# Kernel optimization log

Hardware: AMD Instinct MI355X
Metric: run time of the kernel (lower is better)

## Reference

```python
import jax, jax.numpy as jnp
import numpy as np
import math

N_HEADS = 4
N_ITERS = 2  # SSFormer n=2; each loop iteration recomputes the same values (no feedback in the original code)
BN_EPS = 1e-5


def _attention(q, k, v):
    """SSTransformer: multi-head cross-attention over flattened spatial dims.
    q,k,v: [B, C, H, W] -> returns [B, C, L] with L = H*W.
    """
    b, c = q.shape[0], q.shape[1]
    L = q.shape[2] * q.shape[3]
    ch = c // N_HEADS
    scale = 1.0 / math.sqrt(math.sqrt(ch))
    qf = (q.reshape(b * N_HEADS, ch, L) * scale)
    kf = (k.reshape(b * N_HEADS, ch, L) * scale)
    vf = v.reshape(b * N_HEADS, ch, L)
    # weight: [B*H, t, s]
    w = jnp.einsum('bct,bcs->bts', qf, kf)
    w = jax.nn.softmax(w.astype(jnp.float32), axis=-1).astype(w.dtype)
    a = jnp.einsum('bts,bcs->bct', w, vf)
    return a.reshape(b, c, L)


def setup_inputs() -> dict:
    key = jax.random.key(0)
    k1, k2, k3, k4 = jax.random.split(key, 4)
    B, C, H, W = 8, 512, 32, 32
    c = jax.random.normal(k1, (B, C, H, W), dtype=jnp.float32)
    e = jax.random.normal(k2, (B, C, H, W), dtype=jnp.float32)
    conv_w = jax.random.normal(k3, (C, C, 1, 1), dtype=jnp.float32) / math.sqrt(C)
    conv_b = jax.random.normal(k4, (C,), dtype=jnp.float32) * 0.02
    bn_gamma = jnp.ones((C,), dtype=jnp.float32)
    bn_beta = jnp.zeros((C,), dtype=jnp.float32)
    return {"c": c, "e": e, "conv_w": conv_w, "conv_b": conv_b,
            "bn_gamma": bn_gamma, "bn_beta": bn_beta}


def reference(c, e, conv_w, conv_b, bn_gamma, bn_beta):
    bs, ch, h, w = c.shape
    L = h * w
    for _ in range(N_ITERS):
        _c = _attention(e, c, c)                       # [B, C, L]
        _e = _attention(_c.reshape(bs, ch, h, w), e, e)  # [B, C, L]
    _e = _e.reshape(bs, ch, h, w)
    # Proj: 1x1 conv + BatchNorm2d (training-mode batch stats) + Swish
    x = jnp.einsum('oc,bchw->bohw', conv_w.reshape(ch, ch), _e) + conv_b[None, :, None, None]
    mean = jnp.mean(x, axis=(0, 2, 3), keepdims=True)
    var = jnp.var(x, axis=(0, 2, 3), keepdims=True)
    xn = (x - mean) * jax.lax.rsqrt(var + BN_EPS)
    xn = xn * bn_gamma[None, :, None, None] + bn_beta[None, :, None, None]
    return xn * jax.nn.sigmoid(xn)
```

## Files before the change

### kernel.cpp

```cpp
#include <hip/hip_runtime.h>
#include <hip/hip_bf16.h>

typedef __attribute__((ext_vector_type(8))) short short8;
typedef __attribute__((ext_vector_type(4))) float floatx4;
typedef __attribute__((ext_vector_type(4))) float f32x4;
typedef unsigned short u16;
typedef unsigned int u32;
typedef __attribute__((ext_vector_type(8))) unsigned short ushort8;

#define LSEQ 1024
#define CHD  128
#define QK_SCALE 0.08838834764831845f

static __device__ __forceinline__ u16 f2b(float f) {
  __hip_bfloat16 h = __float2bfloat16(f);
  return *reinterpret_cast<u16*>(&h);
}
static __device__ __forceinline__ u32 pack2(float a, float b) {
  return (u32)f2b(a) | ((u32)f2b(b) << 16);
}
static __device__ __forceinline__ void gl_lds16(const void* g, void* l) {
  __builtin_amdgcn_global_load_lds((__attribute__((address_space(1))) const void*)g,
                                   (__attribute__((address_space(3))) void*)l, 16, 0, 0);
}

__global__ __launch_bounds__(256) void k_prep(const float* __restrict__ in,
                                              u16* __restrict__ outV,
                                              u16* __restrict__ outT) {
  __shared__ u16 tile[32][72];
  int bh = blockIdx.z, c0 = blockIdx.y * 32, s0 = blockIdx.x * 64;
  int tid = threadIdx.x;
  int cl = tid >> 3, sc = tid & 7;
  size_t off = ((size_t)bh * CHD + c0 + cl) * LSEQ + s0 + sc * 8;
  f32x4 a = *(const f32x4*)(in + off);
  f32x4 b = *(const f32x4*)(in + off + 4);
  ushort8 u;
#pragma unroll
  for (int j = 0; j < 4; ++j) { u[j] = f2b(a[j]); u[j + 4] = f2b(b[j]); }
  *(ushort8*)(outV + off) = u;
  *(ushort8*)&tile[cl][sc * 8] = u;
  __syncthreads();
  int sl = tid >> 2, cc = tid & 3;
  ushort8 v;
#pragma unroll
  for (int j = 0; j < 8; ++j) v[j] = tile[cc * 8 + j][sl];
  *(ushort8*)(outT + ((size_t)bh * LSEQ + s0 + sl) * CHD + c0 + cc * 8) = v;
}

__global__ __launch_bounds__(256) void k_wcvt(const float* __restrict__ w, u16* __restrict__ wb,
                                              float* __restrict__ zbuf ) {
  int tid = threadIdx.x;
  int base = (blockIdx.x * 256 + tid) * 8;
  f32x4 a = *(const f32x4*)(w + base);
  f32x4 b = *(const f32x4*)(w + base + 4);
  ushort8 u;
#pragma unroll
  for (int j = 0; j < 4; ++j) { u[j] = f2b(a[j]); u[j + 4] = f2b(b[j]); }
  *(ushort8*)(wb + base) = u;
  if (blockIdx.x == 0) {
    f32x4 z; z[0]=0.f; z[1]=0.f; z[2]=0.f; z[3]=0.f;
    *(f32x4*)(zbuf + tid * 4) = z;
  }
}

__global__ __launch_bounds__(512) void k_attn(const u16* __restrict__ qT,
                                              const u16* __restrict__ kT,
                                              const u16* __restrict__ v,
                                              u16* __restrict__ outT) {
  __shared__ char ldsbuf[81920];

  int bh = blockIdx.x, tt = blockIdx.y;
  int tid = threadIdx.x;
  int w = tid >> 6, lane = tid & 63;
  int lo = lane & 15, hi = lane >> 4;
  int t0 = tt * 128 + w * 16;

  const char* kTb = (const char*)(kT + (size_t)bh * LSEQ * CHD);
  const char* vb  = (const char*)(v  + (size_t)bh * CHD * LSEQ);

  const u16* qbase = qT + ((size_t)bh * LSEQ + t0 + lo) * CHD + hi * 8;
  short8 bq[4];
#pragma unroll
  for (int ks = 0; ks < 4; ++ks) bq[ks] = *(const short8*)(qbase + ks * 32);

  floatx4 oacc[8];
#pragma unroll
  for (int i = 0; i < 8; ++i) { oacc[i][0]=0.f; oacc[i][1]=0.f; oacc[i][2]=0.f; oacc[i][3]=0.f; }
  float m_r = -1e30f, l_r = 0.f;

  char* pw = ldsbuf + 65536 + w * 2048 + lo * 128;
  int sw = (lo & 7) << 4;

  auto stageK = [&](int buf, int sb) {
    char* dst = ldsbuf + buf * 16384;
#pragma unroll
    for (int it = 0; it < 2; ++it) {
      int bb = it * 8192 + tid * 16;
      int row = bb >> 8;
      int cb = (bb & 255) ^ ((row & 7) << 4);
      gl_lds16(kTb + (size_t)(sb * 64 + row) * 256 + cb, dst + bb);
    }
  };
  auto stageV = [&](int buf, int sb) {
    char* dst = ldsbuf + 32768 + buf * 16384;
#pragma unroll
    for (int it = 0; it < 2; ++it) {
      int bb = it * 8192 + tid * 16;
      int row = bb >> 7;
      int cb = (bb & 127) ^ ((row & 7) << 4);
      gl_lds16(vb + (size_t)row * 2048 + sb * 128 + cb, dst + bb);
    }
  };

  stageK(0, 0); stageV(0, 0);
  __syncthreads();
  int cur = 0;

  for (int sb = 0; sb < 16; ++sb) {
    if (sb < 15) { stageK(cur ^ 1, sb + 1); stageV(cur ^ 1, sb + 1); }
    const char* ldsK = ldsbuf + cur * 16384;
    const char* ldsV = ldsbuf + 32768 + cur * 16384;

    float sa[4][4];
#pragma unroll
    for (int ss = 0; ss < 4; ++ss) {
      floatx4 acc; acc[0]=0.f; acc[1]=0.f; acc[2]=0.f; acc[3]=0.f;
      int row = ss * 16 + lo;
#pragma unroll
      for (int ks = 0; ks < 4; ++ks) {
        int cbyte = (ks * 64 + hi * 16) ^ ((row & 7) << 4);
        short8 a = *(const short8*)(ldsK + row * 256 + cbyte);
        acc = __builtin_amdgcn_mfma_f32_16x16x32_bf16(a, bq[ks], acc, 0, 0, 0);
      }
#pragma unroll
      for (int r = 0; r < 4; ++r) sa[ss][r] = acc[r] * QK_SCALE;
    }

    float bm = sa[0][0];
#pragma unroll
    for (int ss = 0; ss < 4; ++ss)
#pragma unroll
      for (int r = 0; r < 4; ++r) bm = fmaxf(bm, sa[ss][r]);
    bm = fmaxf(bm, __shfl_xor(bm, 16));
    bm = fmaxf(bm, __shfl_xor(bm, 32));
    float mn = fmaxf(m_r, bm);
    float corr = __expf(m_r - mn);
    m_r = mn;
    float rs = 0.f;
#pragma unroll
    for (int ss = 0; ss < 4; ++ss)
#pragma unroll
      for (int r = 0; r < 4; ++r) {
        float p = __expf(sa[ss][r] - mn);
        sa[ss][r] = p;
        rs += p;
      }
    rs += __shfl_xor(rs, 16);
    rs += __shfl_xor(rs, 32);
    l_r = l_r * corr + rs;
#pragma unroll
    for (int i = 0; i < 8; ++i) {
      oacc[i][0] *= corr; oacc[i][1] *= corr; oacc[i][2] *= corr; oacc[i][3] *= corr;
    }

#pragma unroll
    for (int ss = 0; ss < 4; ++ss)
#pragma unroll
      for (int r2 = 0; r2 < 2; ++r2) {
        int scol = ss * 16 + hi * 4 + r2 * 2;
        *(u32*)(pw + ((scol * 2) ^ sw)) = pack2(sa[ss][r2 * 2], sa[ss][r2 * 2 + 1]);
      }
    asm volatile("" ::: "memory");

#pragma unroll
    for (int mt = 0; mt < 8; ++mt) {
      int crow = mt * 16 + lo;
      const char* va = ldsV + crow * 128;
      int vsw = (crow & 7) << 4;
#pragma unroll
      for (int k2 = 0; k2 < 2; ++k2) {
        short8 a = *(const short8*)(va + ((k2 * 64 + hi * 16) ^ vsw));
        short8 b = *(const short8*)(pw + ((k2 * 64 + hi * 16) ^ sw));
        oacc[mt] = __builtin_amdgcn_mfma_f32_16x16x32_bf16(a, b, oacc[mt], 0, 0, 0);
      }
    }
    __syncthreads();
    cur ^= 1;
  }

  float inv = 1.0f / l_r;
  char* ot = ldsbuf + w * 4096;
#pragma unroll
  for (int mt = 0; mt < 8; ++mt)
#pragma unroll
    for (int r2 = 0; r2 < 2; ++r2) {
      int cb = (mt * 32 + hi * 8 + r2 * 4) ^ ((lo & 7) << 4);
      *(u32*)(ot + lo * 256 + cb) = pack2(oacc[mt][r2 * 2] * inv, oacc[mt][r2 * 2 + 1] * inv);
    }
  asm volatile("" ::: "memory");
  u16* orow = outT + ((size_t)bh * LSEQ + t0 + lo) * CHD;
#pragma unroll
  for (int it = 0; it < 4; ++it) {
    int cb = (it * 64 + hi * 16) ^ ((lo & 7) << 4);
    ushort8 d = *(const ushort8*)(ot + lo * 256 + cb);
    *(ushort8*)(orow + it * 32 + hi * 8) = d;
  }
}

__global__ __launch_bounds__(256) void k_proj(const u16* __restrict__ Wm,
                                              const u16* __restrict__ eT,
                                              const float* __restrict__ bias,
                                              float* __restrict__ x,
                                              float* __restrict__ chsum,
                                              float* __restrict__ chsq) {
  __shared__ char lds[65536];
  int lt = blockIdx.x, ot = blockIdx.y;
  int b = lt >> 3;
  int l0b = (lt & 7) * 128;
  int o0 = ot * 128;
  int tid = threadIdx.x, w = tid >> 6, lane = tid & 63, lo = lane & 15, hi = lane >> 4;
  int wm = w >> 1, wn = w & 1;
  const char* Wb = (const char*)Wm;
  const char* eTb = (const char*)eT;

  auto stageA = [&](int buf, int kb) {
    char* dst = lds + buf * 16384;
#pragma unroll
    for (int it = 0; it < 4; ++it) {
      int bb = it * 4096 + tid * 16;
      int row = bb >> 7;
      int cb = (bb & 127) ^ ((row & 7) << 4);
      gl_lds16(Wb + (size_t)(o0 + row) * 1024 + kb * 128 + cb, dst + bb);
    }
  };
  auto stageB = [&](int buf, int kb) {
    char* dst = lds + 32768 + buf * 16384;
    int page = b * 4 + (kb >> 1);
    int choff = (kb & 1) * 128;
#pragma unroll
    for (int it = 0; it < 4; ++it) {
      int bb = it * 4096 + tid * 16;
      int row = bb >> 7;
      int cb = (bb & 127) ^ ((row & 7) << 4);
      gl_lds16(eTb + ((size_t)page * 1024 + l0b + row) * 256 + choff + cb, dst + bb);
    }
  };

  floatx4 acc[4][4];
#pragma unroll
  for (int i = 0; i < 4; ++i)
#pragma unroll
    for (int j = 0; j < 4; ++j) { acc[i][j][0]=0.f; acc[i][j][1]=0.f; acc[i][j][2]=0.f; acc[i][j][3]=0.f; }

  stageA(0, 0); stageB(0, 0);
  __syncthreads();
  int cur = 0;

  for (int kb = 0; kb < 8; ++kb) {
    if (kb < 7) { stageA(cur ^ 1, kb + 1); stageB(cur ^ 1, kb + 1); }
    const char* A = lds + cur * 16384;
    const char* B = lds + 32768 + cur * 16384;
#pragma unroll
    for (int kk = 0; kk < 2; ++kk) {
      short8 af[4], bf[4];
#pragma unroll
      for (int mi = 0; mi < 4; ++mi) {
        int row = wm * 64 + mi * 16 + lo;
        af[mi] = *(const short8*)(A + row * 128 + ((kk * 64 + hi * 16) ^ ((row & 7) << 4)));
      }
#pragma unroll
      for (int ni = 0; ni < 4; ++ni) {
        int row = wn * 64 + ni * 16 + lo;
        bf[ni] = *(const short8*)(B + row * 128 + ((kk * 64 + hi * 16) ^ ((row & 7) << 4)));
      }
#pragma unroll
      for (int mi = 0; mi < 4; ++mi)
#pragma unroll
        for (int ni = 0; ni < 4; ++ni)
          acc[mi][ni] = __builtin_amdgcn_mfma_f32_16x16x32_bf16(af[mi], bf[ni], acc[mi][ni], 0, 0, 0);
    }
    __syncthreads();
    cur ^= 1;
  }

#pragma unroll
  for (int mi = 0; mi < 4; ++mi) {
#pragma unroll
    for (int r = 0; r < 4; ++r) {
      int o = o0 + wm * 64 + mi * 16 + hi * 4 + r;
      float bv = bias[o];
      float s = 0.f, q = 0.f;
#pragma unroll
      for (int ni = 0; ni < 4; ++ni) {
        float xv = acc[mi][ni][r] + bv;
        x[((size_t)b * 512 + o) * LSEQ + l0b + wn * 64 + ni * 16 + lo] = xv;
        s += xv; q += xv * xv;
      }
#pragma unroll
      for (int d = 1; d < 16; d <<= 1) { s += __shfl_xor(s, d); q += __shfl_xor(q, d); }
      if (lo == 0) {
        atomicAdd(&chsum[o], s);
        atomicAdd(&chsq[o], q);
      }
    }
  }
}

__global__ void k_stats(const float* __restrict__ chsum, const float* __restrict__ chsq,
                        const float* __restrict__ gamma, const float* __restrict__ beta,
                        float* __restrict__ scale, float* __restrict__ shift) {
  int ch = blockIdx.x * 256 + threadIdx.x;
  if (ch < 512) {
    const float invn = 1.0f / 8192.0f;
    float mean = chsum[ch] * invn;
    float var = chsq[ch] * invn - mean * mean;
    float rstd = rsqrtf(var + 1e-5f);
    float g = gamma[ch] * rstd;
    scale[ch] = g;
    shift[ch] = beta[ch] - mean * g;
  }
}

__global__ __launch_bounds__(256) void k_final(const float* __restrict__ x,
                                               const float* __restrict__ scale,
                                               const float* __restrict__ shift,
                                               float* __restrict__ out) {
  int idx = blockIdx.x * 256 + threadIdx.x;
  int base = idx * 4;
  int ch = (base >> 10) & 511;
  float sc = scale[ch], sh = shift[ch];
  f32x4 vx = *(const f32x4*)(x + base);
  f32x4 o;
#pragma unroll
  for (int j = 0; j < 4; ++j) {
    float xn = vx[j] * sc + sh;
    float sg = 1.0f / (1.0f + __expf(-xn));
    o[j] = xn * sg;
  }
  *(f32x4*)(out + base) = o;
}

extern "C" void kernel_launch(void* const* d_in, const int* in_sizes, int n_in,
                              void* d_out, int out_size, void* d_ws, size_t ws_size,
                              hipStream_t stream) {
  const float* c     = (const float*)d_in[0];
  const float* e     = (const float*)d_in[1];
  const float* Wf    = (const float*)d_in[2];
  const float* bias  = (const float*)d_in[3];
  const float* gamma = (const float*)d_in[4];
  const float* beta  = (const float*)d_in[5];
  float* outp = (float*)d_out;

  char* ws = (char*)d_ws;
  const size_t TB = (size_t)32 * 1024 * 128 * 2;
  u16* eT  = (u16*)(ws);
  u16* cT  = (u16*)(ws + TB);
  u16* cV  = (u16*)(ws + 2 * TB);
  u16* eV  = (u16*)(ws + 3 * TB);
  u16* cT2 = (u16*)(ws + 4 * TB);
  u16* Wbf = (u16*)(ws + 5 * TB);
  float* chsum = (float*)(ws + 5 * TB + (1 << 20));
  float* chsq  = chsum + 512;
  float* scale = chsq + 512;
  float* shift = scale + 512;
  float* x     = (float*)(ws + 2 * TB);

  dim3 tb(256);
  dim3 pgrid(16, 4, 32);
  dim3 agrid(32, 8);

  k_wcvt<<<dim3(128), tb, 0, stream>>>(Wf, Wbf, chsum);
  k_prep<<<pgrid, tb, 0, stream>>>(c, cV, cT);
  k_prep<<<pgrid, tb, 0, stream>>>(e, eV, eT);
  k_attn<<<agrid, dim3(512), 0, stream>>>(eT, cT, cV, cT2);
  k_attn<<<agrid, dim3(512), 0, stream>>>(cT2, eT, eV, cT);
  k_proj<<<dim3(64, 4), tb, 0, stream>>>(Wbf, cT, bias, x, chsum, chsq);
  k_stats<<<dim3(2), tb, 0, stream>>>(chsum, chsq, gamma, beta, scale, shift);
  k_final<<<dim3(4096), tb, 0, stream>>>(x, scale, shift, outp);
}
```

Baseline: 116.5 us.

## Fuse both attention passes into one kernel and merge prep and stats launches

Both cross-attention passes now run inside one kernel. Each block keeps the first pass's normalized output in LDS and reuses it directly as the query of the second pass, since the query rows it needs are exactly the ones it just produced. This removes a global round-trip and a launch. Blocks shrink from 512 to 256 threads with 64 query rows each, giving twice as many blocks. The two prep launches are merged into one grid, the stats kernel is folded into the final elementwise kernel (every thread recomputes its channel's scale and shift), and s_setprio hints are added around the MFMA sections. The tradeoff is fewer queries per block, so each K/V tile staged from global memory is shared by fewer rows, plus a serial dependency between the two passes inside each block.

Measured after the change: 119.1 us. 1.02x slower.

```diff
diff --git a/kernel.cpp b/kernel.cpp
--- a/kernel.cpp
+++ b/kernel.cpp
@@ -24,11 +24,16 @@
                                    (__attribute__((address_space(3))) void*)l, 16, 0, 0);
 }
 
-__global__ __launch_bounds__(256) void k_prep(const float* __restrict__ in,
-                                              u16* __restrict__ outV,
-                                              u16* __restrict__ outT) {
+__global__ __launch_bounds__(256) void k_prep(const float* __restrict__ cin,
+                                              const float* __restrict__ ein,
+                                              u16* __restrict__ cV, u16* __restrict__ cT,
+                                              u16* __restrict__ eV, u16* __restrict__ eT) {
   __shared__ u16 tile[32][72];
-  int bh = blockIdx.z, c0 = blockIdx.y * 32, s0 = blockIdx.x * 64;
+  int z = blockIdx.z;
+  const float* in = (z < 32) ? cin : ein;
+  u16* outV = (z < 32) ? cV : eV;
+  u16* outT = (z < 32) ? cT : eT;
+  int bh = z & 31, c0 = blockIdx.y * 32, s0 = blockIdx.x * 64;
   int tid = threadIdx.x;
   int cl = tid >> 3, sc = tid & 7;
   size_t off = ((size_t)bh * CHD + c0 + cl) * LSEQ + s0 + sc * 8;
@@ -63,130 +68,159 @@
   }
 }
 
-__global__ __launch_bounds__(512) void k_attn(const u16* __restrict__ qT,
-                                              const u16* __restrict__ kT,
-                                              const u16* __restrict__ v,
+__global__ __launch_bounds__(256) void k_attn(const u16* __restrict__ eT,
+                                              const u16* __restrict__ cT,
+                                              const u16* __restrict__ cV,
+                                              const u16* __restrict__ eV,
                                               u16* __restrict__ outT) {
-  __shared__ char ldsbuf[81920];
+  __shared__ char ldsbuf[73728];
 
   int bh = blockIdx.x, tt = blockIdx.y;
   int tid = threadIdx.x;
   int w = tid >> 6, lane = tid & 63;
   int lo = lane & 15, hi = lane >> 4;
-  int t0 = tt * 128 + w * 16;
-
-  const char* kTb = (const char*)(kT + (size_t)bh * LSEQ * CHD);
-  const char* vb  = (const char*)(v  + (size_t)bh * CHD * LSEQ);
-
-  const u16* qbase = qT + ((size_t)bh * LSEQ + t0 + lo) * CHD + hi * 8;
-  short8 bq[4];
-#pragma unroll
-  for (int ks = 0; ks < 4; ++ks) bq[ks] = *(const short8*)(qbase + ks * 32);
-
-  floatx4 oacc[8];
-#pragma unroll
-  for (int i = 0; i < 8; ++i) { oacc[i][0]=0.f; oacc[i][1]=0.f; oacc[i][2]=0.f; oacc[i][3]=0.f; }
-  float m_r = -1e30f, l_r = 0.f;
+  int t0 = tt * 64 + w * 16;
 
   char* pw = ldsbuf + 65536 + w * 2048 + lo * 128;
   int sw = (lo & 7) << 4;
 
-  auto stageK = [&](int buf, int sb) {
+  auto stageK = [&](int buf, int sb, const char* kTb) {
     char* dst = ldsbuf + buf * 16384;
 #pragma unroll
-    for (int it = 0; it < 2; ++it) {
-      int bb = it * 8192 + tid * 16;
+    for (int it = 0; it < 4; ++it) {
+      int bb = it * 4096 + tid * 16;
       int row = bb >> 8;
       int cb = (bb & 255) ^ ((row & 7) << 4);
       gl_lds16(kTb + (size_t)(sb * 64 + row) * 256 + cb, dst + bb);
     }
   };
-  auto stageV = [&](int buf, int sb) {
+  auto stageV = [&](int buf, int sb, const char* vb) {
     char* dst = ldsbuf + 32768 + buf * 16384;
 #pragma unroll
-    for (int it = 0; it < 2; ++it) {
-      int bb = it * 8192 + tid * 16;
+    for (int it = 0; it < 4; ++it) {
+      int bb = it * 4096 + tid * 16;
       int row = bb >> 7;
       int cb = (bb & 127) ^ ((row & 7) << 4);
       gl_lds16(vb + (size_t)row * 2048 + sb * 128 + cb, dst + bb);
     }
   };
 
-  stageK(0, 0); stageV(0, 0);
+  short8 bq[4];
+  floatx4 oacc[8];
+  float m_r, l_r;
+
+  auto flash = [&](const char* kTb, const char* vb) {
+    m_r = -1e30f; l_r = 0.f;
+#pragma unroll
+    for (int i = 0; i < 8; ++i) { oacc[i][0]=0.f; oacc[i][1]=0.f; oacc[i][2]=0.f; oacc[i][3]=0.f; }
+    stageK(0, 0, kTb); stageV(0, 0, vb);
+    __syncthreads();
+    int cur = 0;
+    for (int sb = 0; sb < 16; ++sb) {
+      if (sb < 15) { stageK(cur ^ 1, sb + 1, kTb); stageV(cur ^ 1, sb + 1, vb); }
+      const char* ldsK = ldsbuf + cur * 16384;
+      const char* ldsV = ldsbuf + 32768 + cur * 16384;
+
+      float sa[4][4];
+      __builtin_amdgcn_s_setprio(1);
+#pragma unroll
+      for (int ss = 0; ss < 4; ++ss) {
+        floatx4 acc; acc[0]=0.f; acc[1]=0.f; acc[2]=0.f; acc[3]=0.f;
+        int row = ss * 16 + lo;
+#pragma unroll
+        for (int ks = 0; ks < 4; ++ks) {
+          int cbyte = (ks * 64 + hi * 16) ^ ((row & 7) << 4);
+          short8 a = *(const short8*)(ldsK + row * 256 + cbyte);
+          acc = __builtin_amdgcn_mfma_f32_16x16x32_bf16(a, bq[ks], acc, 0, 0, 0);
+        }
+#pragma unroll
+        for (int r = 0; r < 4; ++r) sa[ss][r] = acc[r] * QK_SCALE;
+      }
+      __builtin_amdgcn_s_setprio(0);
+
+      float bm = sa[0][0];
+#pragma unroll
+      for (int ss = 0; ss < 4; ++ss)
+#pragma unroll
+        for (int r = 0; r < 4; ++r) bm = fmaxf(bm, sa[ss][r]);
+      bm = fmaxf(bm, __shfl_xor(bm, 16));
+      bm = fmaxf(bm, __shfl_xor(bm, 32));
+      float mn = fmaxf(m_r, bm);
+      float corr = __expf(m_r - mn);
+      m_r = mn;
+      float rs = 0.f;
+#pragma unroll
+      for (int ss = 0; ss < 4; ++ss)
+#pragma unroll
+        for (int r = 0; r < 4; ++r) {
+          float p = __expf(sa[ss][r] - mn);
+          sa[ss][r] = p;
+          rs += p;
+        }
+      rs += __shfl_xor(rs, 16);
+      rs += __shfl_xor(rs, 32);
+      l_r = l_r * corr + rs;
+#pragma unroll
+      for (int i = 0; i < 8; ++i) {
+        oacc[i][0] *= corr; oacc[i][1] *= corr; oacc[i][2] *= corr; oacc[i][3] *= corr;
+      }
+
+#pragma unroll
+      for (int ss = 0; ss < 4; ++ss)
+#pragma unroll
+        for (int r2 = 0; r2 < 2; ++r2) {
+          int scol = ss * 16 + hi * 4 + r2 * 2;
+          *(u32*)(pw + ((scol * 2) ^ sw)) = pack2(sa[ss][r2 * 2], sa[ss][r2 * 2 + 1]);
+        }
+      asm volatile("" ::: "memory");
+
+      __builtin_amdgcn_s_setprio(1);
+#pragma unroll
+      for (int mt = 0; mt < 8; ++mt) {
+        int crow = mt * 16 + lo;
+        const char* va = ldsV + crow * 128;
+        int vsw = (crow & 7) << 4;
+#pragma unroll
+        for (int k2 = 0; k2 < 2; ++k2) {
+          short8 a = *(const short8*)(va + ((k2 * 64 + hi * 16) ^ vsw));
+          short8 b = *(const short8*)(pw + ((k2 * 64 + hi * 16) ^ sw));
+          oacc[mt] = __builtin_amdgcn_mfma_f32_16x16x32_bf16(a, b, oacc[mt], 0, 0, 0);
+        }
+      }
+      __builtin_amdgcn_s_setprio(0);
+      __syncthreads();
+      cur ^= 1;
+    }
+  };
+
+  const u16* qbase = eT + ((size_t)bh * LSEQ + t0 + lo) * CHD + hi * 8;
+#pragma unroll
+  for (int ks = 0; ks < 4; ++ks) bq[ks] = *(const short8*)(qbase + ks * 32);
+
+  flash((const char*)(cT + (size_t)bh * LSEQ * CHD),
+        (const char*)(cV + (size_t)bh * CHD * LSEQ));
+
+  {
+    float inv = 1.0f / l_r;
+    char* ot = ldsbuf + w * 4096;
+#pragma unroll
+    for (int mt = 0; mt < 8; ++mt)
+#pragma unroll
+      for (int r2 = 0; r2 < 2; ++r2) {
+        int cb = (mt * 32 + hi * 8 + r2 * 4) ^ ((lo & 7) << 4);
+        *(u32*)(ot + lo * 256 + cb) = pack2(oacc[mt][r2 * 2] * inv, oacc[mt][r2 * 2 + 1] * inv);
+      }
+    asm volatile("" ::: "memory");
+#pragma unroll
+    for (int ks = 0; ks < 4; ++ks) {
+      int cb = (ks * 64 + hi * 16) ^ ((lo & 7) << 4);
+      bq[ks] = *(const short8*)(ot + lo * 256 + cb);
+    }
+  }
   __syncthreads();
-  int cur = 0;
-
-  for (int sb = 0; sb < 16; ++sb) {
-    if (sb < 15) { stageK(cur ^ 1, sb + 1); stageV(cur ^ 1, sb + 1); }
-    const char* ldsK = ldsbuf + cur * 16384;
-    const char* ldsV = ldsbuf + 32768 + cur * 16384;
-
-    float sa[4][4];
-#pragma unroll
-    for (int ss = 0; ss < 4; ++ss) {
-      floatx4 acc; acc[0]=0.f; acc[1]=0.f; acc[2]=0.f; acc[3]=0.f;
-      int row = ss * 16 + lo;
-#pragma unroll
-      for (int ks = 0; ks < 4; ++ks) {
-        int cbyte = (ks * 64 + hi * 16) ^ ((row & 7) << 4);
-        short8 a = *(const short8*)(ldsK + row * 256 + cbyte);
-        acc = __builtin_amdgcn_mfma_f32_16x16x32_bf16(a, bq[ks], acc, 0, 0, 0);
-      }
-#pragma unroll
-      for (int r = 0; r < 4; ++r) sa[ss][r] = acc[r] * QK_SCALE;
-    }
-
-    float bm = sa[0][0];
-#pragma unroll
-    for (int ss = 0; ss < 4; ++ss)
-#pragma unroll
-      for (int r = 0; r < 4; ++r) bm = fmaxf(bm, sa[ss][r]);
-    bm = fmaxf(bm, __shfl_xor(bm, 16));
-    bm = fmaxf(bm, __shfl_xor(bm, 32));
-    float mn = fmaxf(m_r, bm);
-    float corr = __expf(m_r - mn);
-    m_r = mn;
-    float rs = 0.f;
-#pragma unroll
-    for (int ss = 0; ss < 4; ++ss)
-#pragma unroll
-      for (int r = 0; r < 4; ++r) {
-        float p = __expf(sa[ss][r] - mn);
-        sa[ss][r] = p;
-        rs += p;
-      }
-    rs += __shfl_xor(rs, 16);
-    rs += __shfl_xor(rs, 32);
-    l_r = l_r * corr + rs;
-#pragma unroll
-    for (int i = 0; i < 8; ++i) {
-      oacc[i][0] *= corr; oacc[i][1] *= corr; oacc[i][2] *= corr; oacc[i][3] *= corr;
-    }
-
-#pragma unroll
-    for (int ss = 0; ss < 4; ++ss)
-#pragma unroll
-      for (int r2 = 0; r2 < 2; ++r2) {
-        int scol = ss * 16 + hi * 4 + r2 * 2;
-        *(u32*)(pw + ((scol * 2) ^ sw)) = pack2(sa[ss][r2 * 2], sa[ss][r2 * 2 + 1]);
-      }
-    asm volatile("" ::: "memory");
-
-#pragma unroll
-    for (int mt = 0; mt < 8; ++mt) {
-      int crow = mt * 16 + lo;
-      const char* va = ldsV + crow * 128;
-      int vsw = (crow & 7) << 4;
-#pragma unroll
-      for (int k2 = 0; k2 < 2; ++k2) {
-        short8 a = *(const short8*)(va + ((k2 * 64 + hi * 16) ^ vsw));
-        short8 b = *(const short8*)(pw + ((k2 * 64 + hi * 16) ^ sw));
-        oacc[mt] = __builtin_amdgcn_mfma_f32_16x16x32_bf16(a, b, oacc[mt], 0, 0, 0);
-      }
-    }
-    __syncthreads();
-    cur ^= 1;
-  }
+
+  flash((const char*)(eT + (size_t)bh * LSEQ * CHD),
+        (const char*)(eV + (size_t)bh * CHD * LSEQ));
 
   float inv = 1.0f / l_r;
   char* ot = ldsbuf + w * 4096;
@@ -273,11 +307,13 @@
         int row = wn * 64 + ni * 16 + lo;
         bf[ni] = *(const short8*)(B + row * 128 + ((kk * 64 + hi * 16) ^ ((row & 7) << 4)));
       }
+      __builtin_amdgcn_s_setprio(1);
 #pragma unroll
       for (int mi = 0; mi < 4; ++mi)
 #pragma unroll
         for (int ni = 0; ni < 4; ++ni)
           acc[mi][ni] = __builtin_amdgcn_mfma_f32_16x16x32_bf16(af[mi], bf[ni], acc[mi][ni], 0, 0, 0);
+      __builtin_amdgcn_s_setprio(0);
     }
     __syncthreads();
     cur ^= 1;
@@ -306,29 +342,21 @@
   }
 }
 
-__global__ void k_stats(const float* __restrict__ chsum, const float* __restrict__ chsq,
-                        const float* __restrict__ gamma, const float* __restrict__ beta,
-                        float* __restrict__ scale, float* __restrict__ shift) {
-  int ch = blockIdx.x * 256 + threadIdx.x;
-  if (ch < 512) {
-    const float invn = 1.0f / 8192.0f;
-    float mean = chsum[ch] * invn;
-    float var = chsq[ch] * invn - mean * mean;
-    float rstd = rsqrtf(var + 1e-5f);
-    float g = gamma[ch] * rstd;
-    scale[ch] = g;
-    shift[ch] = beta[ch] - mean * g;
-  }
-}
-
 __global__ __launch_bounds__(256) void k_final(const float* __restrict__ x,
-                                               const float* __restrict__ scale,
-                                               const float* __restrict__ shift,
+                                               const float* __restrict__ chsum,
+                                               const float* __restrict__ chsq,
+                                               const float* __restrict__ gamma,
+                                               const float* __restrict__ beta,
                                                float* __restrict__ out) {
   int idx = blockIdx.x * 256 + threadIdx.x;
   int base = idx * 4;
   int ch = (base >> 10) & 511;
-  float sc = scale[ch], sh = shift[ch];
+  const float invn = 1.0f / 8192.0f;
+  float mean = chsum[ch] * invn;
+  float var = chsq[ch] * invn - mean * mean;
+  float rstd = rsqrtf(var + 1e-5f);
+  float sc = gamma[ch] * rstd;
+  float sh = beta[ch] - mean * sc;
   f32x4 vx = *(const f32x4*)(x + base);
   f32x4 o;
 #pragma unroll
@@ -357,24 +385,17 @@
   u16* cT  = (u16*)(ws + TB);
   u16* cV  = (u16*)(ws + 2 * TB);
   u16* eV  = (u16*)(ws + 3 * TB);
-  u16* cT2 = (u16*)(ws + 4 * TB);
+  u16* xT  = (u16*)(ws + 4 * TB);
   u16* Wbf = (u16*)(ws + 5 * TB);
   float* chsum = (float*)(ws + 5 * TB + (1 << 20));
   float* chsq  = chsum + 512;
-  float* scale = chsq + 512;
-  float* shift = scale + 512;
-  float* x     = (float*)(ws + 2 * TB);
+  float* x     = (float*)(ws + 6 * TB);
 
   dim3 tb(256);
-  dim3 pgrid(16, 4, 32);
-  dim3 agrid(32, 8);
 
   k_wcvt<<<dim3(128), tb, 0, stream>>>(Wf, Wbf, chsum);
-  k_prep<<<pgrid, tb, 0, stream>>>(c, cV, cT);
-  k_prep<<<pgrid, tb, 0, stream>>>(e, eV, eT);
-  k_attn<<<agrid, dim3(512), 0, stream>>>(eT, cT, cV, cT2);
-  k_attn<<<agrid, dim3(512), 0, stream>>>(cT2, eT, eV, cT);
-  k_proj<<<dim3(64, 4), tb, 0, stream>>>(Wbf, cT, bias, x, chsum, chsq);
-  k_stats<<<dim3(2), tb, 0, stream>>>(chsum, chsq, gamma, beta, scale, shift);
-  k_final<<<dim3(4096), tb, 0, stream>>>(x, scale, shift, outp);
-}
+  k_prep<<<dim3(16, 4, 64), tb, 0, stream>>>(c, e, cV, cT, eV, eT);
+  k_attn<<<dim3(32, 16), tb, 0, stream>>>(eT, cT, cV, eV, xT);
+  k_proj<<<dim3(64, 4), tb, 0, stream>>>(Wbf, xT, bias, x, chsum, chsq);
+  k_final<<<dim3(4096), tb, 0, stream>>>(x, chsum, chsq, gamma, beta, outp);
+}
```
